# Performance work log

Measured on AMD Instinct MI355X. Metric: run time of the kernel, lower is better.

Reference implementation:

```python
import math
import jax, jax.numpy as jnp
import numpy as np

FACIL_RATE = 2.0
FIRE_THRESH = 0.85
MAX_GATE = 8.0
EPS = 1e-12  # F.normalize eps

B, T, D = 8, 4096, 2048


def _gelu(x):
    # tanh-approx GELU, exactly as in the torch module
    c = math.sqrt(2.0 / math.pi)
    return 0.5 * x * (1.0 + jnp.tanh(c * (x + 0.044715 * x * x * x)))


def _l2norm(v, axis=-1):
    n = jnp.sqrt(jnp.sum(v * v, axis=axis, keepdims=True))
    return v / jnp.maximum(n, EPS)


def setup_inputs() -> dict:
    key = jax.random.key(0)
    k1, k2 = jax.random.split(key)
    x = jax.random.normal(k1, (B, T, D), dtype=jnp.float32)
    pos_buf = jax.random.normal(k2, (T, D), dtype=jnp.float32)
    pos_facil = jnp.ones((T,), dtype=jnp.float32)
    log_k_pos = jnp.asarray(math.log(0.5), dtype=jnp.float32)
    return {"x": x, "log_k_pos": log_k_pos, "pos_buf": pos_buf, "pos_facil": pos_facil}


def reference(x, log_k_pos, pos_buf, pos_facil):
    # steady-state (pass1 complete) path of GELU275.forward
    k_pos = jnp.clip(jnp.exp(log_k_pos), 0.01, 5.0)
    y = _gelu(x)                                   # [B,T,D]
    # everything below the gelu except the final gate multiply runs under
    # no_grad / on y.detach() in torch -> stop_gradient here
    y_det = jax.lax.stop_gradient(y)
    pos_buf_n = _l2norm(jax.lax.stop_gradient(pos_buf))          # [T,D]
    y_n = _l2norm(y_det)                                          # [B,T,D]
    sim = jnp.einsum("btd,td->bt", y_n, pos_buf_n)               # cosine sim [B,T]
    fire_mask = jnp.mean(sim, axis=0) > FIRE_THRESH              # [T]
    pf = jax.lax.stop_gradient(pos_facil)
    facil_t = jnp.where(fire_mask, jnp.minimum(pf * FACIL_RATE, 16.0), pf)  # [T]
    gate = jnp.minimum(1.0 + k_pos * (facil_t[None, :] - 1.0) * sim, MAX_GATE)  # [B,T]
    return y * gate[:, :, None]
```

## Files before the change

kernel.cpp:

```cpp
#include <hip/hip_runtime.h>
#include <math.h>

#define BB 8
#define TT 4096
#define DD 2048
#define HALF 1024
#define THREADS 512
#define NT 8
#define NBLK (TT / NT)
#define NG (NT * 2)
#define SMEM_BYTES ((2 * BB * HALF + 2 * HALF) * 4)

typedef float v4f __attribute__((ext_vector_type(4)));

__device__ __forceinline__ float gelu_fast(float x) {
    const float c1 = 1.5957691216057308f;
    const float c2 = 0.07135481282556483f;
    float e = __expf(-x * fmaf(c2, x * x, c1));
    return x * __builtin_amdgcn_rcpf(1.0f + e);
}

__device__ __forceinline__ void gl2lds16(const float* g, float* l) {
    __builtin_amdgcn_global_load_lds(
        (const __attribute__((address_space(1))) void*)g,
        (__attribute__((address_space(3))) void*)l, 16, 0, 0);
}
__device__ __forceinline__ void gl2lds4(const float* g, float* l) {
    __builtin_amdgcn_global_load_lds(
        (const __attribute__((address_space(1))) void*)g,
        (__attribute__((address_space(3))) void*)l, 4, 0, 0);
}

__global__ __launch_bounds__(THREADS, 4) void gelu275_fused(
    const float* __restrict__ x,
    const float* __restrict__ log_k_pos,
    const float* __restrict__ pos_buf,
    const float* __restrict__ pos_facil,
    float* __restrict__ out)
{
    extern __shared__ __align__(16) float smem[];
    float* const xbuf0 = smem;
    float* const xbuf1 = smem + BB * HALF;
    float* const pbuf0 = smem + 2 * BB * HALF;
    float* const pbuf1 = pbuf0 + HALF;
    __shared__ float s_red[17];

    const int tid  = threadIdx.x;
    const int lane = tid & 63;
    const int wave = tid >> 6;
    const int t0   = blockIdx.x * NT;
    const int base = lane * 4;

    const float kp = fminf(fmaxf(__expf(log_k_pos[0]), 0.01f), 5.0f);
    float pfv[NT];
#pragma unroll
    for (int i = 0; i < NT; ++i) pfv[i] = pos_facil[t0 + i];

    const float* xrow = x       + ((size_t)wave * TT + t0) * DD;
    const float* prow = pos_buf + (size_t)t0 * DD;
    float*       orow = out     + ((size_t)wave * TT + t0) * DD;

    {
#pragma unroll
        for (int c = 0; c < 4; ++c)
            gl2lds16(xrow + c * 256 + base, xbuf0 + wave * HALF + c * 256);
        gl2lds4(prow + wave * 128 + lane,      pbuf0 + wave * 128);
        gl2lds4(prow + wave * 128 + 64 + lane, pbuf0 + wave * 128 + 64);
    }

    v4f Y[8];
    float dot = 0.f, yn2 = 0.f, pn2 = 0.f;

#pragma unroll
    for (int g = 0; g < NG; ++g) {
        const int tloc = g >> 1;
        const int h    = g & 1;
        float* const xc = h ? xbuf1 : xbuf0;
        float* const pc = h ? pbuf1 : pbuf0;

        if (g + 1 < NG) {
            const int tn = (g + 1) >> 1;
            const int hn = (g + 1) & 1;
            float* const xn = hn ? xbuf1 : xbuf0;
            float* const pn = hn ? pbuf1 : pbuf0;
            const float* xs = xrow + (size_t)tn * DD + hn * HALF;
            const float* pp = prow + (size_t)tn * DD + hn * HALF;
#pragma unroll
            for (int c = 0; c < 4; ++c)
                gl2lds16(xs + c * 256 + base, xn + wave * HALF + c * 256);
            gl2lds4(pp + wave * 128 + lane,      pn + wave * 128);
            gl2lds4(pp + wave * 128 + 64 + lane, pn + wave * 128 + 64);
        }

        if (g == 0)           { asm volatile("s_waitcnt vmcnt(6)"  ::: "memory"); }
        else if (g == NG - 1) { asm volatile("s_waitcnt vmcnt(0)"  ::: "memory"); }
        else if (h == 0)      { asm volatile("s_waitcnt vmcnt(14)" ::: "memory"); }
        else                  { asm volatile("s_waitcnt vmcnt(6)"  ::: "memory"); }
        __builtin_amdgcn_s_barrier();
        asm volatile("" ::: "memory");

        if (h == 0) { dot = 0.f; yn2 = 0.f; pn2 = 0.f; }
#pragma unroll
        for (int c = 0; c < 4; ++c) {
            v4f v       = *(const v4f*)(xc + wave * HALF + c * 256 + base);
            const v4f p = *(const v4f*)(pc + c * 256 + base);
            v.x = gelu_fast(v.x); v.y = gelu_fast(v.y);
            v.z = gelu_fast(v.z); v.w = gelu_fast(v.w);
            Y[h * 4 + c] = v;
            dot += v.x * p.x + v.y * p.y + v.z * p.z + v.w * p.w;
            yn2 += v.x * v.x + v.y * v.y + v.z * v.z + v.w * v.w;
            pn2 += p.x * p.x + p.y * p.y + p.z * p.z + p.w * p.w;
        }

        if (h == 1) {
#pragma unroll
            for (int off = 32; off; off >>= 1) {
                dot += __shfl_xor(dot, off);
                yn2 += __shfl_xor(yn2, off);
                pn2 += __shfl_xor(pn2, off);
            }
            if (lane == 0) {
                s_red[wave]     = dot;
                s_red[8 + wave] = yn2;
                if (wave == 0) s_red[16] = pn2;
            }
        }

        asm volatile("s_waitcnt lgkmcnt(0)" ::: "memory");
        __builtin_amdgcn_s_barrier();
        asm volatile("" ::: "memory");

        if (h == 1) {
            const float pnn = fmaxf(sqrtf(s_red[16]), 1e-12f);
            float simsum = 0.f, simw = 0.f;
#pragma unroll
            for (int bb = 0; bb < BB; ++bb) {
                const float s = s_red[bb] *
                    __builtin_amdgcn_rcpf(
                        fmaxf(sqrtf(s_red[8 + bb]), 1e-12f) * pnn);
                simsum += s;
                if (bb == wave) simw = s;
            }
            const bool  fire  = (simsum * 0.125f) > 0.85f;
            const float pf    = pfv[tloc];
            const float facil = fire ? fminf(pf * 2.0f, 16.0f) : pf;
            const float gt    = fminf(1.0f + kp * (facil - 1.0f) * simw, 8.0f);

            float* o = orow + (size_t)tloc * DD;
#pragma unroll
            for (int k = 0; k < 8; ++k) {
                v4f ov = Y[k];
                ov.x *= gt; ov.y *= gt; ov.z *= gt; ov.w *= gt;
                *(v4f*)(o + (k >> 2) * HALF + (k & 3) * 256 + base) = ov;
            }
        }
    }
}

extern "C" void kernel_launch(void* const* d_in, const int* in_sizes, int n_in,
                              void* d_out, int out_size, void* d_ws, size_t ws_size,
                              hipStream_t stream) {
    const float* x          = (const float*)d_in[0];
    const float* log_k_pos  = (const float*)d_in[1];
    const float* pos_buf    = (const float*)d_in[2];
    const float* pos_facil  = (const float*)d_in[3];
    float* out              = (float*)d_out;

    (void)hipFuncSetAttribute((const void*)gelu275_fused,
                              hipFuncAttributeMaxDynamicSharedMemorySize,
                              SMEM_BYTES);

    dim3 grid(NBLK);
    dim3 block(THREADS);
    gelu275_fused<<<grid, block, SMEM_BYTES, stream>>>(
        x, log_k_pos, pos_buf, pos_facil, out);
}
```

Before: 120.6 us.

## Split rows into quarter-chunks to halve LDS and double block occupancy

Each pipeline stage now stages a quarter row (512 floats) instead of half, which halves the shared-memory footprint to about 36 KB. Blocks handle 4 timesteps instead of 8, so the grid doubles, and launch bounds ask for 8 blocks per CU. The goal is more resident waves to hide memory latency. In exchange there are more barriers per row and smaller in-flight loads per wave, and pos_facil is now loaded where it is used instead of being prefetched.

```diff
diff --git a/kernel.cpp b/kernel.cpp
--- a/kernel.cpp
+++ b/kernel.cpp
@@ -4,12 +4,12 @@
 #define BB 8
 #define TT 4096
 #define DD 2048
-#define HALF 1024
+#define QF 512
 #define THREADS 512
-#define NT 8
+#define NT 4
 #define NBLK (TT / NT)
-#define NG (NT * 2)
-#define SMEM_BYTES ((2 * BB * HALF + 2 * HALF) * 4)
+#define NG (NT * 4)
+#define SMEM_BYTES ((2 * BB * QF + 2 * QF) * 4)
 
 typedef float v4f __attribute__((ext_vector_type(4)));
 
@@ -31,7 +31,7 @@
         (__attribute__((address_space(3))) void*)l, 4, 0, 0);
 }
 
-__global__ __launch_bounds__(THREADS, 4) void gelu275_fused(
+__global__ __launch_bounds__(THREADS, 8) void gelu275_fused(
     const float* __restrict__ x,
     const float* __restrict__ log_k_pos,
     const float* __restrict__ pos_buf,
@@ -39,10 +39,10 @@
     float* __restrict__ out)
 {
     extern __shared__ __align__(16) float smem[];
-    float* const xbuf0 = smem;
-    float* const xbuf1 = smem + BB * HALF;
-    float* const pbuf0 = smem + 2 * BB * HALF;
-    float* const pbuf1 = pbuf0 + HALF;
+    float* const xb0 = smem;
+    float* const xb1 = smem + BB * QF;
+    float* const pb0 = smem + 2 * BB * QF;
+    float* const pb1 = pb0 + QF;
     __shared__ float s_red[17];
 
     const int tid  = threadIdx.x;
@@ -52,67 +52,57 @@
     const int base = lane * 4;
 
     const float kp = fminf(fmaxf(__expf(log_k_pos[0]), 0.01f), 5.0f);
-    float pfv[NT];
-#pragma unroll
-    for (int i = 0; i < NT; ++i) pfv[i] = pos_facil[t0 + i];
 
     const float* xrow = x       + ((size_t)wave * TT + t0) * DD;
     const float* prow = pos_buf + (size_t)t0 * DD;
     float*       orow = out     + ((size_t)wave * TT + t0) * DD;
 
-    {
-#pragma unroll
-        for (int c = 0; c < 4; ++c)
-            gl2lds16(xrow + c * 256 + base, xbuf0 + wave * HALF + c * 256);
-        gl2lds4(prow + wave * 128 + lane,      pbuf0 + wave * 128);
-        gl2lds4(prow + wave * 128 + 64 + lane, pbuf0 + wave * 128 + 64);
-    }
+    gl2lds16(xrow + base,        xb0 + wave * QF);
+    gl2lds16(xrow + 256 + base,  xb0 + wave * QF + 256);
+    gl2lds4 (prow + wave * 64 + lane, pb0 + wave * 64);
 
     v4f Y[8];
     float dot = 0.f, yn2 = 0.f, pn2 = 0.f;
 
 #pragma unroll
     for (int g = 0; g < NG; ++g) {
-        const int tloc = g >> 1;
-        const int h    = g & 1;
-        float* const xc = h ? xbuf1 : xbuf0;
-        float* const pc = h ? pbuf1 : pbuf0;
+        const int tl = g >> 2;
+        const int q  = g & 3;
+        float* const xc = (g & 1) ? xb1 : xb0;
+        float* const pc = (g & 1) ? pb1 : pb0;
 
         if (g + 1 < NG) {
-            const int tn = (g + 1) >> 1;
-            const int hn = (g + 1) & 1;
-            float* const xn = hn ? xbuf1 : xbuf0;
-            float* const pn = hn ? pbuf1 : pbuf0;
-            const float* xs = xrow + (size_t)tn * DD + hn * HALF;
-            const float* pp = prow + (size_t)tn * DD + hn * HALF;
-#pragma unroll
-            for (int c = 0; c < 4; ++c)
-                gl2lds16(xs + c * 256 + base, xn + wave * HALF + c * 256);
-            gl2lds4(pp + wave * 128 + lane,      pn + wave * 128);
-            gl2lds4(pp + wave * 128 + 64 + lane, pn + wave * 128 + 64);
+            const int   gn = g + 1;
+            float* const xn = (gn & 1) ? xb1 : xb0;
+            float* const pn = (gn & 1) ? pb1 : pb0;
+            const float* xs = xrow + (size_t)(gn >> 2) * DD + (gn & 3) * QF;
+            const float* ps = prow + (size_t)(gn >> 2) * DD + (gn & 3) * QF;
+            gl2lds16(xs + base,       xn + wave * QF);
+            gl2lds16(xs + 256 + base, xn + wave * QF + 256);
+            gl2lds4 (ps + wave * 64 + lane, pn + wave * 64);
         }
 
-        if (g == 0)           { asm volatile("s_waitcnt vmcnt(6)"  ::: "memory"); }
+        if (g == 0)           { asm volatile("s_waitcnt vmcnt(3)"  ::: "memory"); }
         else if (g == NG - 1) { asm volatile("s_waitcnt vmcnt(0)"  ::: "memory"); }
-        else if (h == 0)      { asm volatile("s_waitcnt vmcnt(14)" ::: "memory"); }
-        else                  { asm volatile("s_waitcnt vmcnt(6)"  ::: "memory"); }
+        else if (q == 0)      { asm volatile("s_waitcnt vmcnt(11)" ::: "memory"); }
+        else                  { asm volatile("s_waitcnt vmcnt(3)"  ::: "memory"); }
         __builtin_amdgcn_s_barrier();
         asm volatile("" ::: "memory");
 
-        if (h == 0) { dot = 0.f; yn2 = 0.f; pn2 = 0.f; }
+        if (q == 0) { dot = 0.f; yn2 = 0.f; pn2 = 0.f; }
 #pragma unroll
-        for (int c = 0; c < 4; ++c) {
-            v4f v       = *(const v4f*)(xc + wave * HALF + c * 256 + base);
+        for (int c = 0; c < 2; ++c) {
+            v4f v       = *(const v4f*)(xc + wave * QF + c * 256 + base);
             const v4f p = *(const v4f*)(pc + c * 256 + base);
             v.x = gelu_fast(v.x); v.y = gelu_fast(v.y);
             v.z = gelu_fast(v.z); v.w = gelu_fast(v.w);
-            Y[h * 4 + c] = v;
+            Y[q * 2 + c] = v;
             dot += v.x * p.x + v.y * p.y + v.z * p.z + v.w * p.w;
             yn2 += v.x * v.x + v.y * v.y + v.z * v.z + v.w * v.w;
             pn2 += p.x * p.x + p.y * p.y + p.z * p.z + p.w * p.w;
         }
 
-        if (h == 1) {
+        if (q == 3) {
 #pragma unroll
             for (int off = 32; off; off >>= 1) {
                 dot += __shfl_xor(dot, off);
@@ -130,7 +120,7 @@
         __builtin_amdgcn_s_barrier();
         asm volatile("" ::: "memory");
 
-        if (h == 1) {
+        if (q == 3) {
             const float pnn = fmaxf(sqrtf(s_red[16]), 1e-12f);
             float simsum = 0.f, simw = 0.f;
 #pragma unroll
@@ -142,16 +132,16 @@
                 if (bb == wave) simw = s;
             }
             const bool  fire  = (simsum * 0.125f) > 0.85f;
-            const float pf    = pfv[tloc];
+            const float pf    = pos_facil[t0 + tl];
             const float facil = fire ? fminf(pf * 2.0f, 16.0f) : pf;
             const float gt    = fminf(1.0f + kp * (facil - 1.0f) * simw, 8.0f);
 
-            float* o = orow + (size_t)tloc * DD;
+            float* o = orow + (size_t)tl * DD;
 #pragma unroll
             for (int k = 0; k < 8; ++k) {
                 v4f ov = Y[k];
                 ov.x *= gt; ov.y *= gt; ov.z *= gt; ov.w *= gt;
-                *(v4f*)(o + (k >> 2) * HALF + (k & 3) * 256 + base) = ov;
+                *(v4f*)(o + (k >> 1) * QF + (k & 1) * 256 + base) = ov;
             }
         }
     }
@@ -166,10 +156,6 @@
     const float* pos_facil  = (const float*)d_in[3];
     float* out              = (float*)d_out;
 
-    (void)hipFuncSetAttribute((const void*)gelu275_fused,
-                              hipFuncAttributeMaxDynamicSharedMemorySize,
-                              SMEM_BYTES);
-
     dim3 grid(NBLK);
     dim3 block(THREADS);
     gelu275_fused<<<grid, block, SMEM_BYTES, stream>>>(
```

Result: slower. 145.3 us (+20.5%).
